# Kernel tuning notes

Hardware: AMD Instinct MI355X
Metric: run time of the kernel (lower is better)

The kernel has to match this reference:

```python
import jax, jax.numpy as jnp
from jax import lax
import numpy as np

INPUT_SIZE = 128
NUM_FRAMES = 4
NUM_OBJECTS = 32
DN = ('NCHW', 'OIHW', 'NCHW')


def _conv(x, w, b):
    y = lax.conv_general_dilated(x, w, window_strides=(1, 1), padding='SAME',
                                 dimension_numbers=DN)
    return y + b[None, :, None, None]


def setup_inputs() -> dict:
    key = jax.random.key(0)
    k = jax.random.split(key, 6)
    B = 32
    images = jax.random.uniform(k[0], (B, NUM_FRAMES, 3, INPUT_SIZE, INPUT_SIZE), jnp.float32) * 255.0
    rois = jax.random.randint(k[1], (B, INPUT_SIZE, INPUT_SIZE), 0, NUM_OBJECTS, jnp.int32)
    conv1_w = jax.random.normal(k[2], (64, 3 * NUM_FRAMES, 3, 3), jnp.float32) * 0.05
    conv1_b = jnp.zeros((64,), jnp.float32)
    conv2_w = jax.random.normal(k[3], (128, 64, 3, 3), jnp.float32) * 0.05
    conv2_b = jnp.zeros((128,), jnp.float32)
    return {'images': images, 'rois': rois, 'conv1_w': conv1_w, 'conv1_b': conv1_b,
            'conv2_w': conv2_w, 'conv2_b': conv2_b}


def reference(images, rois, conv1_w, conv1_b, conv2_w, conv2_b):
    B = images.shape[0]
    # backbone: conv -> relu -> maxpool2x2 -> conv -> relu
    x = images.reshape(B, 3 * NUM_FRAMES, INPUT_SIZE, INPUT_SIZE) / 255.0
    x = jax.nn.relu(_conv(x, conv1_w, conv1_b))
    x = lax.reduce_window(x, -jnp.inf, lax.max, (1, 1, 2, 2), (1, 1, 2, 2), 'VALID')
    x = jax.nn.relu(_conv(x, conv2_w, conv2_b))  # (B, 128, 64, 64)
    C = x.shape[1]
    # roi_pool: one-hot(rois) nearest-downsampled to 64x64, broadcast-multiply,
    # max over H,W == per-id segment max (x >= 0 post-relu; absent id -> 0)
    ids = rois[:, ::2, ::2].reshape(B, -1)
    feat = x.reshape(B, C, -1).transpose(0, 2, 1)  # (B, HW, C)

    def pool_one(f, i):  # f: (HW, C), i: (HW,)
        return jax.ops.segment_max(f, i, num_segments=NUM_OBJECTS)  # (O, C)

    pooled = jax.vmap(pool_one)(feat, ids)  # (B, O, C)
    return jnp.maximum(pooled, 0.0)
```

## Files before the change

kernel.cpp:

```cpp
#include <hip/hip_runtime.h>

#define IN 128
#define PD 64
#define C1 64
#define C2 128
#define ICC 12
#define NOBJ 32
#define PADW 66

typedef __attribute__((ext_vector_type(8))) short bf16x8;
typedef __attribute__((ext_vector_type(4))) float f32x4;

static __device__ __forceinline__ unsigned short f2bf(float f) {
  unsigned u = __float_as_uint(f);
  return (unsigned short)((u + 0x7FFFu + ((u >> 16) & 1u)) >> 16);
}

__global__ __launch_bounds__(256) void k0_pack_w1(
    const float* __restrict__ w1, unsigned short* __restrict__ wp)
{
  int i = blockIdx.x * 256 + threadIdx.x;
  if (i < 10 * C1 * 16) {
    int tap = i >> 10;
    int rem = i & 1023;
    int oc = rem >> 4, ch = rem & 15;
    float v = (tap < 9 && ch < ICC) ? w1[((size_t)oc * ICC + ch) * 9 + tap] : 0.f;
    wp[i] = f2bf(v);
  }
}

__global__ __launch_bounds__(512, 4) void k1_mfma(
    const float* __restrict__ img, const unsigned short* __restrict__ wp1,
    const float* __restrict__ b1, const float* __restrict__ w2,
    unsigned short* __restrict__ wq, unsigned short* __restrict__ xpad)
{
  const int t = threadIdx.x;

  if (blockIdx.y == 32) {
    for (int j = blockIdx.x * 512 + t; j < 9 * C2 * C1; j += 64 * 512) {
      const int tmp = j / 9, tap = j - tmp * 9;
      const int ic = tmp & 63, oc = tmp >> 6;
      const int k2 = ic >> 5, l16 = (ic >> 3) & 3, e = ic & 7;
      const int ocb = oc >> 4, l15 = oc & 15;
      wq[((tap * 2 + k2) * 8 + ocb) * 512 + l16 * 128 + l15 * 8 + e] = f2bf(w2[j]);
    }
    return;
  }

  const int l = t & 63, w = t >> 6;
  const int wm = w >> 1, wn = w & 1;
  const int bx = blockIdx.x & 7, by = blockIdx.x >> 3;
  const int b  = blockIdx.y;
  const int l15 = l & 15, l16 = l >> 4;

  __shared__ uint4 xs4[324 * 3];

  if (t < 324) {
    unsigned int* xu = reinterpret_cast<unsigned int*>(xs4);
    xu[t * 12 + 6] = 0;
    xu[t * 12 + 7] = 0;
  }

  const float* imgb = img + ((size_t)b * ICC << 14);
  float v0[4], v1[4];
  int   dpix[4], dcp[4];
#pragma unroll
  for (int it = 0; it < 4; ++it) {
    const int i = t + it * 512;
    const bool ok = i < 1944;
    const int cp  = ok ? (i / 324) : 0;
    const int pix = i - cp * 324;
    const int y = (pix * 57) >> 10;
    const int x = pix - y * 18;
    const int iy = by * 16 + y - 1, ix = bx * 16 + x - 1;
    dpix[it] = pix; dcp[it] = cp;
    v0[it] = 0.f; v1[it] = 0.f;
    if (ok && iy >= 0 && iy < IN && ix >= 0 && ix < IN) {
      const float* p0 = imgb + ((size_t)(2 * cp) << 14) + iy * IN + ix;
      v0[it] = p0[0];
      v1[it] = p0[16384];
    }
  }
#pragma unroll
  for (int it = 0; it < 4; ++it) {
    if (t + it * 512 < 1944) {
      unsigned short h0 = f2bf(v0[it] * (1.f / 255.f));
      unsigned short h1 = f2bf(v1[it] * (1.f / 255.f));
      reinterpret_cast<unsigned int*>(xs4)[dpix[it] * 12 + dcp[it]] =
          (unsigned int)h0 | ((unsigned int)h1 << 16);
    }
  }
  __syncthreads();

  f32x4 acc[4][2];
#pragma unroll
  for (int mf = 0; mf < 4; ++mf)
#pragma unroll
    for (int nf = 0; nf < 2; ++nf) acc[mf][nf] = (f32x4){0.f, 0.f, 0.f, 0.f};

  const char* xs_raw = reinterpret_cast<const char*>(xs4);
  const int ck = l16 & 1;
#pragma unroll
  for (int kp = 0; kp < 5; ++kp) {
    const int ta = 2 * kp, tb = 2 * kp + 1;
    const int tbA = (tb > 8) ? 8 : tb;
    const int dya = ta / 3, dxa = ta % 3;
    const int dyb = tbA / 3, dxb = tbA % 3;
    const int dy = (l16 < 2) ? dya : dyb;
    const int dx = (l16 < 2) ? dxa : dxb;
    const int tw = (l16 < 2) ? ta : tb;

    bf16x8 a[4], bw[2];
#pragma unroll
    for (int mf = 0; mf < 4; ++mf) {
      const int row = wm * 4 + mf;
      const int s = (row + dy) * 18 + (l15 + dx);
      a[mf] = *reinterpret_cast<const bf16x8*>(xs_raw + s * 48 + ck * 16);
    }
#pragma unroll
    for (int nf = 0; nf < 2; ++nf) {
      const int oc = wn * 32 + nf * 16 + l15;
      bw[nf] = *reinterpret_cast<const bf16x8*>(wp1 + ((tw * C1 + oc) * 16 + ck * 8));
    }
#pragma unroll
    for (int mf = 0; mf < 4; ++mf)
#pragma unroll
      for (int nf = 0; nf < 2; ++nf)
        acc[mf][nf] = __builtin_amdgcn_mfma_f32_16x16x32_bf16(
            a[mf], bw[nf], acc[mf][nf], 0, 0, 0);
  }

  float bias[2];
#pragma unroll
  for (int nf = 0; nf < 2; ++nf) bias[nf] = b1[wn * 32 + nf * 16 + l15];

#pragma unroll
  for (int q = 0; q < 2; ++q) {
    const int gy = by * 8 + wm * 2 + q;
    unsigned short* orow = xpad + (((size_t)b * PADW + (gy + 1)) * PADW + 1) * C1;
#pragma unroll
    for (int nf = 0; nf < 2; ++nf) {
      const int oc = wn * 32 + nf * 16 + l15;
      const f32x4 A0 = acc[2 * q][nf], A1 = acc[2 * q + 1][nf];
      const float p0 = fmaxf(fmaxf(A0[0], A0[1]), fmaxf(A1[0], A1[1]));
      const float p1 = fmaxf(fmaxf(A0[2], A0[3]), fmaxf(A1[2], A1[3]));
      const float v0s = fmaxf(p0 + bias[nf], 0.f);
      const float v1s = fmaxf(p1 + bias[nf], 0.f);
      const int gx0 = bx * 8 + l16 * 2;
      orow[(size_t)gx0 * C1 + oc]       = f2bf(v0s);
      orow[(size_t)(gx0 + 1) * C1 + oc] = f2bf(v1s);
    }
  }
}

__global__ __launch_bounds__(256) void k2_mfma(
    const unsigned short* __restrict__ xpad, const unsigned short* __restrict__ wq,
    const float* __restrict__ b2, const int* __restrict__ rois,
    float* __restrict__ part)
{
  const int t  = threadIdx.x;
  const int l  = t & 63, w = t >> 6;
  const int wm = w >> 1, wn = w & 1;
  const int bx = blockIdx.x & 3, by = blockIdx.x >> 2;
  const int b  = blockIdx.y;
  const int l15 = l & 15, l16 = l >> 4;

  __shared__ uint4 xs4[180 * 8];
  __shared__ int   smax[NOBJ * 132];
  __shared__ int   ids_s[128];

  const unsigned short* xb = xpad + (size_t)b * PADW * PADW * C1;
  uint4 sv[6];
#pragma unroll
  for (int it = 0; it < 6; ++it) {
    const int i = t + it * 256;
    const bool ok = i < 1440;
    const int r = i >> 3, ps = i & 7;
    const int y = (r * 57) >> 10;
    const int x = r - y * 18;
    const int cl = ps ^ (r & 7);
    const int gy = by * 8 + y, gx = bx * 16 + x;
    sv[it] = make_uint4(0, 0, 0, 0);
    if (ok && gy >= 1 && gy <= PD && gx >= 1 && gx <= PD)
      sv[it] = *(reinterpret_cast<const uint4*>(xb + ((size_t)gy * PADW + gx) * C1) + cl);
  }
#pragma unroll
  for (int it = 0; it < 6; ++it)
    if (t + it * 256 < 1440) xs4[t + it * 256] = sv[it];

  if (t < 128) {
    const int py = t >> 4, pxx = t & 15;
    ids_s[t] = rois[((size_t)b * IN + 2 * (by * 8 + py)) * IN + 2 * (bx * 16 + pxx)];
  }
  {
    uint4* sm4 = reinterpret_cast<uint4*>(smax);
    const uint4 z = make_uint4(0, 0, 0, 0);
#pragma unroll
    for (int i = 0; i < 5; ++i) {
      const int j = t + i * 256;
      if (j < 1056) sm4[j] = z;
    }
  }
  __syncthreads();

  f32x4 acc[4][4];
#pragma unroll
  for (int mf = 0; mf < 4; ++mf)
#pragma unroll
    for (int nf = 0; nf < 4; ++nf) acc[mf][nf] = (f32x4){0.f, 0.f, 0.f, 0.f};

  const char* xs_raw = reinterpret_cast<const char*>(xs4);

  bf16x8 aR[2][4], bR[2][4];
#pragma unroll
  for (int mf = 0; mf < 4; ++mf) {
    const int m_loc = wm * 64 + mf * 16 + l15;
    const int s = (m_loc >> 4) * 18 + (m_loc & 15);
    const int c = l16 ^ (s & 7);
    aR[0][mf] = *reinterpret_cast<const bf16x8*>(xs_raw + s * 128 + c * 16);
  }
#pragma unroll
  for (int nf = 0; nf < 4; ++nf)
    bR[0][nf] = *reinterpret_cast<const bf16x8*>(
        wq + ((size_t)(wn * 4 + nf)) * 512 + l * 8);

#pragma unroll
  for (int st = 0; st < 18; ++st) {
    const int cur = st & 1, nxt = cur ^ 1;
    if (st < 17) {
      const int s1 = st + 1;
      const int tap1 = s1 >> 1, k21 = s1 & 1;
      const int kr1 = tap1 / 3, kc1 = tap1 % 3;
#pragma unroll
      for (int nf = 0; nf < 4; ++nf)
        bR[nxt][nf] = *reinterpret_cast<const bf16x8*>(
            wq + ((size_t)((tap1 * 2 + k21) * 8 + wn * 4 + nf)) * 512 + l * 8);
#pragma unroll
      for (int mf = 0; mf < 4; ++mf) {
        const int m_loc = wm * 64 + mf * 16 + l15;
        const int s = ((m_loc >> 4) + kr1) * 18 + ((m_loc & 15) + kc1);
        const int c = (k21 * 4 + l16) ^ (s & 7);
        aR[nxt][mf] = *reinterpret_cast<const bf16x8*>(xs_raw + s * 128 + c * 16);
      }
    }
#pragma unroll
    for (int mf = 0; mf < 4; ++mf)
#pragma unroll
      for (int nf = 0; nf < 4; ++nf)
        acc[mf][nf] = __builtin_amdgcn_mfma_f32_16x16x32_bf16(
            aR[cur][mf], bR[cur][nf], acc[mf][nf], 0, 0, 0);
  }

  float bias[4];
#pragma unroll
  for (int nf = 0; nf < 4; ++nf) bias[nf] = b2[wn * 64 + nf * 16 + l15];

#pragma unroll
  for (int mf = 0; mf < 4; ++mf) {
#pragma unroll
    for (int reg = 0; reg < 4; ++reg) {
      const int m_loc = wm * 64 + mf * 16 + l16 * 4 + reg;
      const int id = ids_s[m_loc];
#pragma unroll
      for (int nf = 0; nf < 4; ++nf) {
        const int oc = wn * 64 + nf * 16 + l15;
        const float val = fmaxf(acc[mf][nf][reg] + bias[nf], 0.f);
        atomicMax(&smax[id * 132 + oc], __float_as_int(val));
      }
    }
  }
  __syncthreads();

  uint4* pb4 = reinterpret_cast<uint4*>(part + ((size_t)b * 32 + blockIdx.x) * (NOBJ * C2));
  const uint4* sm4 = reinterpret_cast<const uint4*>(smax);
#pragma unroll
  for (int i = 0; i < 4; ++i) {
    const int j = t + i * 256;
    const int row = j >> 5, c4 = j & 31;
    pb4[j] = sm4[row * 33 + c4];
  }
}

__global__ __launch_bounds__(256) void k3_reduce(
    const float* __restrict__ part, float* __restrict__ out)
{
  const int idx = blockIdx.x * 256 + threadIdx.x;
  const int b = idx >> 12, slot = idx & 4095;
  const float* p = part + (size_t)b * 32 * 4096 + slot;
  float m = 0.f;
#pragma unroll
  for (int tl = 0; tl < 32; ++tl) m = fmaxf(m, p[tl * 4096]);
  out[idx] = m;
}

extern "C" void kernel_launch(void* const* d_in, const int* in_sizes, int n_in,
                              void* d_out, int out_size, void* d_ws, size_t ws_size,
                              hipStream_t stream)
{
  (void)in_sizes; (void)n_in; (void)ws_size; (void)out_size;
  const float* images = (const float*)d_in[0];
  const int*   rois   = (const int*)d_in[1];
  const float* w1     = (const float*)d_in[2];
  const float* b1     = (const float*)d_in[3];
  const float* w2     = (const float*)d_in[4];
  const float* b2     = (const float*)d_in[5];

  const size_t xpad_bytes = (size_t)32 * PADW * PADW * C1 * 2;
  const size_t wq_bytes   = (size_t)9 * C2 * C1 * 2;
  const size_t wp1_bytes  = (size_t)10 * C1 * 16 * 2;

  unsigned short* xpad = (unsigned short*)d_ws;
  unsigned short* wq   = (unsigned short*)((char*)d_ws + xpad_bytes);
  unsigned short* wp1  = (unsigned short*)((char*)d_ws + xpad_bytes + wq_bytes);
  float* part = (float*)((char*)d_ws + xpad_bytes + wq_bytes + wp1_bytes);

  hipLaunchKernelGGL(k0_pack_w1, dim3(40), dim3(256), 0, stream, w1, wp1);

  hipLaunchKernelGGL(k1_mfma, dim3(64, 33), dim3(512), 0, stream,
                     images, wp1, b1, w2, wq, xpad);

  hipLaunchKernelGGL(k2_mfma, dim3(32, 32), dim3(256), 0, stream,
                     xpad, wq, b2, rois, part);

  hipLaunchKernelGGL(k3_reduce, dim3(512), dim3(256), 0, stream,
                     part, (float*)d_out);
}
```

Before: 56.51 us.

## Switch both conv MFMA kernels from 16x16x32 to 32x32x16 bf16 tiles

Both convolution kernels now use the 32x32x16 bf16 MFMA instruction instead of 16x16x32, and the packed weight layouts for conv1 and conv2 are reorganised to match the new operand fragments. Conv1 now does one tap per K-step, dropping the old paired-tap trick and its padding tap. Conv2 runs 36 smaller K-steps with fewer fragments per wave. The intent is fewer LDS operand loads and MFMA issues per output tile, at the cost of redoing the accumulator-to-pixel mapping used by the pooling and atomic-max epilogues.

```diff
diff --git a/kernel.cpp b/kernel.cpp
--- a/kernel.cpp
+++ b/kernel.cpp
@@ -9,7 +9,7 @@
 #define PADW 66
 
 typedef __attribute__((ext_vector_type(8))) short bf16x8;
-typedef __attribute__((ext_vector_type(4))) float f32x4;
+typedef __attribute__((ext_vector_type(16))) float f32x16;
 
 static __device__ __forceinline__ unsigned short f2bf(float f) {
   unsigned u = __float_as_uint(f);
@@ -19,13 +19,13 @@
 __global__ __launch_bounds__(256) void k0_pack_w1(
     const float* __restrict__ w1, unsigned short* __restrict__ wp)
 {
-  int i = blockIdx.x * 256 + threadIdx.x;
-  if (i < 10 * C1 * 16) {
-    int tap = i >> 10;
-    int rem = i & 1023;
-    int oc = rem >> 4, ch = rem & 15;
-    float v = (tap < 9 && ch < ICC) ? w1[((size_t)oc * ICC + ch) * 9 + tap] : 0.f;
-    wp[i] = f2bf(v);
+  int j = blockIdx.x * 256 + threadIdx.x;
+  if (j < 9 * 2 * 64 * 8) {
+    const int e = j & 7, lane = (j >> 3) & 63, ocb = (j >> 9) & 1, tap = j >> 10;
+    const int oc = ocb * 32 + (lane & 31);
+    const int ch = (lane >> 5) * 8 + e;
+    float v = (ch < ICC) ? w1[((size_t)oc * ICC + ch) * 9 + tap] : 0.f;
+    wp[j] = f2bf(v);
   }
 }
 
@@ -40,9 +40,11 @@
     for (int j = blockIdx.x * 512 + t; j < 9 * C2 * C1; j += 64 * 512) {
       const int tmp = j / 9, tap = j - tmp * 9;
       const int ic = tmp & 63, oc = tmp >> 6;
-      const int k2 = ic >> 5, l16 = (ic >> 3) & 3, e = ic & 7;
-      const int ocb = oc >> 4, l15 = oc & 15;
-      wq[((tap * 2 + k2) * 8 + ocb) * 512 + l16 * 128 + l15 * 8 + e] = f2bf(w2[j]);
+      const int s  = tap * 4 + (ic >> 4);
+      const int kk = ic & 15;
+      const int lane = ((kk >> 3) << 5) | (oc & 31);
+      const int ocb  = oc >> 5;
+      wq[((s * 4 + ocb) << 9) + lane * 8 + (kk & 7)] = f2bf(w2[j]);
     }
     return;
   }
@@ -51,7 +53,7 @@
   const int wm = w >> 1, wn = w & 1;
   const int bx = blockIdx.x & 7, by = blockIdx.x >> 3;
   const int b  = blockIdx.y;
-  const int l15 = l & 15, l16 = l >> 4;
+  const int l31 = l & 31, h = l >> 5;
 
   __shared__ uint4 xs4[324 * 3];
 
@@ -92,63 +94,42 @@
   }
   __syncthreads();
 
-  f32x4 acc[4][2];
-#pragma unroll
-  for (int mf = 0; mf < 4; ++mf)
-#pragma unroll
-    for (int nf = 0; nf < 2; ++nf) acc[mf][nf] = (f32x4){0.f, 0.f, 0.f, 0.f};
+  f32x16 acc[2];
+#pragma unroll
+  for (int mf = 0; mf < 2; ++mf)
+#pragma unroll
+    for (int e = 0; e < 16; ++e) acc[mf][e] = 0.f;
 
   const char* xs_raw = reinterpret_cast<const char*>(xs4);
-  const int ck = l16 & 1;
-#pragma unroll
-  for (int kp = 0; kp < 5; ++kp) {
-    const int ta = 2 * kp, tb = 2 * kp + 1;
-    const int tbA = (tb > 8) ? 8 : tb;
-    const int dya = ta / 3, dxa = ta % 3;
-    const int dyb = tbA / 3, dxb = tbA % 3;
-    const int dy = (l16 < 2) ? dya : dyb;
-    const int dx = (l16 < 2) ? dxa : dxb;
-    const int tw = (l16 < 2) ? ta : tb;
-
-    bf16x8 a[4], bw[2];
-#pragma unroll
-    for (int mf = 0; mf < 4; ++mf) {
-      const int row = wm * 4 + mf;
-      const int s = (row + dy) * 18 + (l15 + dx);
-      a[mf] = *reinterpret_cast<const bf16x8*>(xs_raw + s * 48 + ck * 16);
-    }
-#pragma unroll
-    for (int nf = 0; nf < 2; ++nf) {
-      const int oc = wn * 32 + nf * 16 + l15;
-      bw[nf] = *reinterpret_cast<const bf16x8*>(wp1 + ((tw * C1 + oc) * 16 + ck * 8));
-    }
-#pragma unroll
-    for (int mf = 0; mf < 4; ++mf)
-#pragma unroll
-      for (int nf = 0; nf < 2; ++nf)
-        acc[mf][nf] = __builtin_amdgcn_mfma_f32_16x16x32_bf16(
-            a[mf], bw[nf], acc[mf][nf], 0, 0, 0);
-  }
-
-  float bias[2];
-#pragma unroll
-  for (int nf = 0; nf < 2; ++nf) bias[nf] = b1[wn * 32 + nf * 16 + l15];
-
-#pragma unroll
-  for (int q = 0; q < 2; ++q) {
-    const int gy = by * 8 + wm * 2 + q;
+#pragma unroll
+  for (int tap = 0; tap < 9; ++tap) {
+    const int dy = tap / 3, dx = tap % 3;
+    bf16x8 bw = *reinterpret_cast<const bf16x8*>(wp1 + (((tap * 2 + wn) << 9) + l * 8));
+    bf16x8 a[2];
+#pragma unroll
+    for (int mf = 0; mf < 2; ++mf) {
+      const int m  = wm * 64 + mf * 32 + l31;
+      const int s  = ((m >> 4) + dy) * 18 + ((m & 15) + dx);
+      a[mf] = *reinterpret_cast<const bf16x8*>(xs_raw + s * 48 + h * 16);
+    }
+#pragma unroll
+    for (int mf = 0; mf < 2; ++mf)
+      acc[mf] = __builtin_amdgcn_mfma_f32_32x32x16_bf16(a[mf], bw, acc[mf], 0, 0, 0);
+  }
+
+  const int oc = wn * 32 + l31;
+  const float bias0 = b1[oc];
+#pragma unroll
+  for (int mf = 0; mf < 2; ++mf) {
+    const int gy = by * 8 + wm * 2 + mf;
     unsigned short* orow = xpad + (((size_t)b * PADW + (gy + 1)) * PADW + 1) * C1;
 #pragma unroll
-    for (int nf = 0; nf < 2; ++nf) {
-      const int oc = wn * 32 + nf * 16 + l15;
-      const f32x4 A0 = acc[2 * q][nf], A1 = acc[2 * q + 1][nf];
-      const float p0 = fmaxf(fmaxf(A0[0], A0[1]), fmaxf(A1[0], A1[1]));
-      const float p1 = fmaxf(fmaxf(A0[2], A0[3]), fmaxf(A1[2], A1[3]));
-      const float v0s = fmaxf(p0 + bias[nf], 0.f);
-      const float v1s = fmaxf(p1 + bias[nf], 0.f);
-      const int gx0 = bx * 8 + l16 * 2;
-      orow[(size_t)gx0 * C1 + oc]       = f2bf(v0s);
-      orow[(size_t)(gx0 + 1) * C1 + oc] = f2bf(v1s);
+    for (int j = 0; j < 4; ++j) {
+      const float p = fmaxf(fmaxf(acc[mf][2 * j], acc[mf][2 * j + 1]),
+                            fmaxf(acc[mf][2 * j + 8], acc[mf][2 * j + 9]));
+      const float v = fmaxf(p + bias0, 0.f);
+      const int gx = bx * 8 + ((j & 1) | ((j >> 1) << 2)) + 2 * h;
+      orow[(size_t)gx * C1 + oc] = f2bf(v);
     }
   }
 }
@@ -163,7 +144,7 @@
   const int wm = w >> 1, wn = w & 1;
   const int bx = blockIdx.x & 3, by = blockIdx.x >> 2;
   const int b  = blockIdx.y;
-  const int l15 = l & 15, l16 = l >> 4;
+  const int l31 = l & 31, h = l >> 5;
 
   __shared__ uint4 xs4[180 * 8];
   __shared__ int   smax[NOBJ * 132];
@@ -203,67 +184,70 @@
   }
   __syncthreads();
 
-  f32x4 acc[4][4];
-#pragma unroll
-  for (int mf = 0; mf < 4; ++mf)
-#pragma unroll
-    for (int nf = 0; nf < 4; ++nf) acc[mf][nf] = (f32x4){0.f, 0.f, 0.f, 0.f};
+  f32x16 acc[2][2];
+#pragma unroll
+  for (int mf = 0; mf < 2; ++mf)
+#pragma unroll
+    for (int nf = 0; nf < 2; ++nf)
+#pragma unroll
+      for (int e = 0; e < 16; ++e) acc[mf][nf][e] = 0.f;
 
   const char* xs_raw = reinterpret_cast<const char*>(xs4);
 
-  bf16x8 aR[2][4], bR[2][4];
-#pragma unroll
-  for (int mf = 0; mf < 4; ++mf) {
-    const int m_loc = wm * 64 + mf * 16 + l15;
-    const int s = (m_loc >> 4) * 18 + (m_loc & 15);
-    const int c = l16 ^ (s & 7);
-    aR[0][mf] = *reinterpret_cast<const bf16x8*>(xs_raw + s * 128 + c * 16);
-  }
-#pragma unroll
-  for (int nf = 0; nf < 4; ++nf)
+  bf16x8 aR[2][2], bR[2][2];
+#pragma unroll
+  for (int mf = 0; mf < 2; ++mf) {
+    const int m = wm * 64 + mf * 32 + l31;
+    const int sp = (m >> 4) * 18 + (m & 15);
+    const int c = h ^ (sp & 7);
+    aR[0][mf] = *reinterpret_cast<const bf16x8*>(xs_raw + sp * 128 + c * 16);
+  }
+#pragma unroll
+  for (int nf = 0; nf < 2; ++nf)
     bR[0][nf] = *reinterpret_cast<const bf16x8*>(
-        wq + ((size_t)(wn * 4 + nf)) * 512 + l * 8);
-
-#pragma unroll
-  for (int st = 0; st < 18; ++st) {
+        wq + (((size_t)(wn * 2 + nf)) << 9) + l * 8);
+
+#pragma unroll
+  for (int st = 0; st < 36; ++st) {
     const int cur = st & 1, nxt = cur ^ 1;
-    if (st < 17) {
+    if (st < 35) {
       const int s1 = st + 1;
-      const int tap1 = s1 >> 1, k21 = s1 & 1;
+      const int tap1 = s1 >> 2, q1 = s1 & 3;
       const int kr1 = tap1 / 3, kc1 = tap1 % 3;
 #pragma unroll
-      for (int nf = 0; nf < 4; ++nf)
+      for (int nf = 0; nf < 2; ++nf)
         bR[nxt][nf] = *reinterpret_cast<const bf16x8*>(
-            wq + ((size_t)((tap1 * 2 + k21) * 8 + wn * 4 + nf)) * 512 + l * 8);
-#pragma unroll
-      for (int mf = 0; mf < 4; ++mf) {
-        const int m_loc = wm * 64 + mf * 16 + l15;
-        const int s = ((m_loc >> 4) + kr1) * 18 + ((m_loc & 15) + kc1);
-        const int c = (k21 * 4 + l16) ^ (s & 7);
-        aR[nxt][mf] = *reinterpret_cast<const bf16x8*>(xs_raw + s * 128 + c * 16);
+            wq + (((size_t)(s1 * 4 + wn * 2 + nf)) << 9) + l * 8);
+#pragma unroll
+      for (int mf = 0; mf < 2; ++mf) {
+        const int m = wm * 64 + mf * 32 + l31;
+        const int sp = ((m >> 4) + kr1) * 18 + ((m & 15) + kc1);
+        const int c = (q1 * 2 + h) ^ (sp & 7);
+        aR[nxt][mf] = *reinterpret_cast<const bf16x8*>(xs_raw + sp * 128 + c * 16);
       }
     }
 #pragma unroll
-    for (int mf = 0; mf < 4; ++mf)
-#pragma unroll
-      for (int nf = 0; nf < 4; ++nf)
-        acc[mf][nf] = __builtin_amdgcn_mfma_f32_16x16x32_bf16(
+    for (int mf = 0; mf < 2; ++mf)
+#pragma unroll
+      for (int nf = 0; nf < 2; ++nf)
+        acc[mf][nf] = __builtin_amdgcn_mfma_f32_32x32x16_bf16(
             aR[cur][mf], bR[cur][nf], acc[mf][nf], 0, 0, 0);
   }
 
-  float bias[4];
-#pragma unroll
-  for (int nf = 0; nf < 4; ++nf) bias[nf] = b2[wn * 64 + nf * 16 + l15];
-
-#pragma unroll
-  for (int mf = 0; mf < 4; ++mf) {
-#pragma unroll
-    for (int reg = 0; reg < 4; ++reg) {
-      const int m_loc = wm * 64 + mf * 16 + l16 * 4 + reg;
-      const int id = ids_s[m_loc];
-#pragma unroll
-      for (int nf = 0; nf < 4; ++nf) {
-        const int oc = wn * 64 + nf * 16 + l15;
+  float bias[2];
+#pragma unroll
+  for (int nf = 0; nf < 2; ++nf) bias[nf] = b2[wn * 64 + nf * 32 + l31];
+
+#pragma unroll
+  for (int mf = 0; mf < 2; ++mf) {
+#pragma unroll
+    for (int reg = 0; reg < 16; ++reg) {
+      const int row = (reg & 3) + 8 * (reg >> 2) + 4 * h;
+      const int pix = wm * 64 + mf * 32 + row;
+      const int id = ids_s[pix];
+#pragma unroll
+      for (int nf = 0; nf < 2; ++nf) {
+        const int oc = wn * 64 + nf * 32 + l31;
         const float val = fmaxf(acc[mf][nf][reg] + bias[nf], 0.f);
         atomicMax(&smax[id * 132 + oc], __float_as_int(val));
       }
@@ -306,15 +290,15 @@
   const float* b2     = (const float*)d_in[5];
 
   const size_t xpad_bytes = (size_t)32 * PADW * PADW * C1 * 2;
-  const size_t wq_bytes   = (size_t)9 * C2 * C1 * 2;
-  const size_t wp1_bytes  = (size_t)10 * C1 * 16 * 2;
+  const size_t wq_bytes   = (size_t)36 * 4 * 512 * 2;
+  const size_t wp1_bytes  = (size_t)9 * 2 * 512 * 2;
 
   unsigned short* xpad = (unsigned short*)d_ws;
   unsigned short* wq   = (unsigned short*)((char*)d_ws + xpad_bytes);
   unsigned short* wp1  = (unsigned short*)((char*)d_ws + xpad_bytes + wq_bytes);
   float* part = (float*)((char*)d_ws + xpad_bytes + wq_bytes + wp1_bytes);
 
-  hipLaunchKernelGGL(k0_pack_w1, dim3(40), dim3(256), 0, stream, w1, wp1);
+  hipLaunchKernelGGL(k0_pack_w1, dim3(36), dim3(256), 0, stream, w1, wp1);
 
   hipLaunchKernelGGL(k1_mfma, dim3(64, 33), dim3(512), 0, stream,
                      images, wp1, b1, w2, wq, xpad);
```

Result: slower. 61.07 us (+8.1%).

## Process two horizontal tiles per conv1 block with prefetched image loads

Applied to the files above, without the earlier changes.

Each conv1 block now handles two adjacent 16x16 tiles instead of one, so the grid is halved. The global image loads for the second tile are issued before the first tile's MFMA and epilogue, hiding load latency behind compute. The trade-offs are fewer blocks in flight, extra register pressure from holding the prefetched values, and one more barrier per block. The weight-repack stride is adjusted to match the smaller grid.

```diff
diff --git a/kernel.cpp b/kernel.cpp
--- a/kernel.cpp
+++ b/kernel.cpp
@@ -37,7 +37,7 @@
   const int t = threadIdx.x;
 
   if (blockIdx.y == 32) {
-    for (int j = blockIdx.x * 512 + t; j < 9 * C2 * C1; j += 64 * 512) {
+    for (int j = blockIdx.x * 512 + t; j < 9 * C2 * C1; j += 32 * 512) {
       const int tmp = j / 9, tap = j - tmp * 9;
       const int ic = tmp & 63, oc = tmp >> 6;
       const int k2 = ic >> 5, l16 = (ic >> 3) & 3, e = ic & 7;
@@ -49,8 +49,9 @@
 
   const int l = t & 63, w = t >> 6;
   const int wm = w >> 1, wn = w & 1;
-  const int bx = blockIdx.x & 7, by = blockIdx.x >> 3;
-  const int b  = blockIdx.y;
+  const int bxp = (blockIdx.x & 3) << 1;
+  const int by  = blockIdx.x >> 2;
+  const int b   = blockIdx.y;
   const int l15 = l & 15, l16 = l >> 4;
 
   __shared__ uint4 xs4[324 * 3];
@@ -62,95 +63,123 @@
   }
 
   const float* imgb = img + ((size_t)b * ICC << 14);
-  float v0[4], v1[4];
-  int   dpix[4], dcp[4];
-#pragma unroll
-  for (int it = 0; it < 4; ++it) {
-    const int i = t + it * 512;
-    const bool ok = i < 1944;
-    const int cp  = ok ? (i / 324) : 0;
-    const int pix = i - cp * 324;
-    const int y = (pix * 57) >> 10;
-    const int x = pix - y * 18;
-    const int iy = by * 16 + y - 1, ix = bx * 16 + x - 1;
-    dpix[it] = pix; dcp[it] = cp;
-    v0[it] = 0.f; v1[it] = 0.f;
-    if (ok && iy >= 0 && iy < IN && ix >= 0 && ix < IN) {
-      const float* p0 = imgb + ((size_t)(2 * cp) << 14) + iy * IN + ix;
-      v0[it] = p0[0];
-      v1[it] = p0[16384];
-    }
-  }
-#pragma unroll
-  for (int it = 0; it < 4; ++it) {
-    if (t + it * 512 < 1944) {
-      unsigned short h0 = f2bf(v0[it] * (1.f / 255.f));
-      unsigned short h1 = f2bf(v1[it] * (1.f / 255.f));
-      reinterpret_cast<unsigned int*>(xs4)[dpix[it] * 12 + dcp[it]] =
-          (unsigned int)h0 | ((unsigned int)h1 << 16);
-    }
-  }
-  __syncthreads();
-
-  f32x4 acc[4][2];
-#pragma unroll
-  for (int mf = 0; mf < 4; ++mf)
-#pragma unroll
-    for (int nf = 0; nf < 2; ++nf) acc[mf][nf] = (f32x4){0.f, 0.f, 0.f, 0.f};
+
+  auto stage_load = [&](int bx, float (&v0)[4], float (&v1)[4]) {
+#pragma unroll
+    for (int it = 0; it < 4; ++it) {
+      const int i = t + it * 512;
+      const bool ok = i < 1944;
+      const int cp  = ok ? (i / 324) : 0;
+      const int pix = i - cp * 324;
+      const int y = (pix * 57) >> 10;
+      const int x = pix - y * 18;
+      const int iy = by * 16 + y - 1, ix = bx * 16 + x - 1;
+      v0[it] = 0.f; v1[it] = 0.f;
+      if (ok && iy >= 0 && iy < IN && ix >= 0 && ix < IN) {
+        const float* p0 = imgb + ((size_t)(2 * cp) << 14) + iy * IN + ix;
+        v0[it] = p0[0];
+        v1[it] = p0[16384];
+      }
+    }
+  };
+  auto stage_write = [&](const float (&v0)[4], const float (&v1)[4]) {
+#pragma unroll
+    for (int it = 0; it < 4; ++it) {
+      const int i = t + it * 512;
+      if (i < 1944) {
+        const int cp  = i / 324;
+        const int pix = i - cp * 324;
+        unsigned short h0 = f2bf(v0[it] * (1.f / 255.f));
+        unsigned short h1 = f2bf(v1[it] * (1.f / 255.f));
+        reinterpret_cast<unsigned int*>(xs4)[pix * 12 + cp] =
+            (unsigned int)h0 | ((unsigned int)h1 << 16);
+      }
+    }
+  };
 
   const char* xs_raw = reinterpret_cast<const char*>(xs4);
   const int ck = l16 & 1;
-#pragma unroll
-  for (int kp = 0; kp < 5; ++kp) {
-    const int ta = 2 * kp, tb = 2 * kp + 1;
-    const int tbA = (tb > 8) ? 8 : tb;
-    const int dya = ta / 3, dxa = ta % 3;
-    const int dyb = tbA / 3, dxb = tbA % 3;
-    const int dy = (l16 < 2) ? dya : dyb;
-    const int dx = (l16 < 2) ? dxa : dxb;
-    const int tw = (l16 < 2) ? ta : tb;
-
-    bf16x8 a[4], bw[2];
-#pragma unroll
-    for (int mf = 0; mf < 4; ++mf) {
-      const int row = wm * 4 + mf;
-      const int s = (row + dy) * 18 + (l15 + dx);
-      a[mf] = *reinterpret_cast<const bf16x8*>(xs_raw + s * 48 + ck * 16);
-    }
-#pragma unroll
-    for (int nf = 0; nf < 2; ++nf) {
-      const int oc = wn * 32 + nf * 16 + l15;
-      bw[nf] = *reinterpret_cast<const bf16x8*>(wp1 + ((tw * C1 + oc) * 16 + ck * 8));
-    }
-#pragma unroll
-    for (int mf = 0; mf < 4; ++mf)
-#pragma unroll
-      for (int nf = 0; nf < 2; ++nf)
-        acc[mf][nf] = __builtin_amdgcn_mfma_f32_16x16x32_bf16(
-            a[mf], bw[nf], acc[mf][nf], 0, 0, 0);
-  }
+
+  auto do_mfma = [&](f32x4 (&acc)[4][2]) {
+#pragma unroll
+    for (int kp = 0; kp < 5; ++kp) {
+      const int ta = 2 * kp, tb = 2 * kp + 1;
+      const int tbA = (tb > 8) ? 8 : tb;
+      const int dya = ta / 3, dxa = ta % 3;
+      const int dyb = tbA / 3, dxb = tbA % 3;
+      const int dy = (l16 < 2) ? dya : dyb;
+      const int dx = (l16 < 2) ? dxa : dxb;
+      const int tw = (l16 < 2) ? ta : tb;
+
+      bf16x8 a[4], bw[2];
+#pragma unroll
+      for (int mf = 0; mf < 4; ++mf) {
+        const int row = wm * 4 + mf;
+        const int s = (row + dy) * 18 + (l15 + dx);
+        a[mf] = *reinterpret_cast<const bf16x8*>(xs_raw + s * 48 + ck * 16);
+      }
+#pragma unroll
+      for (int nf = 0; nf < 2; ++nf) {
+        const int oc = wn * 32 + nf * 16 + l15;
+        bw[nf] = *reinterpret_cast<const bf16x8*>(wp1 + ((tw * C1 + oc) * 16 + ck * 8));
+      }
+#pragma unroll
+      for (int mf = 0; mf < 4; ++mf)
+#pragma unroll
+        for (int nf = 0; nf < 2; ++nf)
+          acc[mf][nf] = __builtin_amdgcn_mfma_f32_16x16x32_bf16(
+              a[mf], bw[nf], acc[mf][nf], 0, 0, 0);
+    }
+  };
 
   float bias[2];
 #pragma unroll
   for (int nf = 0; nf < 2; ++nf) bias[nf] = b1[wn * 32 + nf * 16 + l15];
 
-#pragma unroll
-  for (int q = 0; q < 2; ++q) {
-    const int gy = by * 8 + wm * 2 + q;
-    unsigned short* orow = xpad + (((size_t)b * PADW + (gy + 1)) * PADW + 1) * C1;
-#pragma unroll
-    for (int nf = 0; nf < 2; ++nf) {
-      const int oc = wn * 32 + nf * 16 + l15;
-      const f32x4 A0 = acc[2 * q][nf], A1 = acc[2 * q + 1][nf];
-      const float p0 = fmaxf(fmaxf(A0[0], A0[1]), fmaxf(A1[0], A1[1]));
-      const float p1 = fmaxf(fmaxf(A0[2], A0[3]), fmaxf(A1[2], A1[3]));
-      const float v0s = fmaxf(p0 + bias[nf], 0.f);
-      const float v1s = fmaxf(p1 + bias[nf], 0.f);
-      const int gx0 = bx * 8 + l16 * 2;
-      orow[(size_t)gx0 * C1 + oc]       = f2bf(v0s);
-      orow[(size_t)(gx0 + 1) * C1 + oc] = f2bf(v1s);
-    }
-  }
+  auto epilogue = [&](int bx, f32x4 (&acc)[4][2]) {
+#pragma unroll
+    for (int q = 0; q < 2; ++q) {
+      const int gy = by * 8 + wm * 2 + q;
+      unsigned short* orow = xpad + (((size_t)b * PADW + (gy + 1)) * PADW + 1) * C1;
+#pragma unroll
+      for (int nf = 0; nf < 2; ++nf) {
+        const int oc = wn * 32 + nf * 16 + l15;
+        const f32x4 A0 = acc[2 * q][nf], A1 = acc[2 * q + 1][nf];
+        const float p0 = fmaxf(fmaxf(A0[0], A0[1]), fmaxf(A1[0], A1[1]));
+        const float p1 = fmaxf(fmaxf(A0[2], A0[3]), fmaxf(A1[2], A1[3]));
+        const float v0s = fmaxf(p0 + bias[nf], 0.f);
+        const float v1s = fmaxf(p1 + bias[nf], 0.f);
+        const int gx0 = bx * 8 + l16 * 2;
+        orow[(size_t)gx0 * C1 + oc]       = f2bf(v0s);
+        orow[(size_t)(gx0 + 1) * C1 + oc] = f2bf(v1s);
+      }
+    }
+  };
+
+  float v0[4], v1[4];
+  f32x4 acc[4][2];
+
+  stage_load(bxp, v0, v1);
+  stage_write(v0, v1);
+  __syncthreads();
+
+  stage_load(bxp + 1, v0, v1);
+#pragma unroll
+  for (int mf = 0; mf < 4; ++mf)
+#pragma unroll
+    for (int nf = 0; nf < 2; ++nf) acc[mf][nf] = (f32x4){0.f, 0.f, 0.f, 0.f};
+  do_mfma(acc);
+  epilogue(bxp, acc);
+  __syncthreads();
+
+  stage_write(v0, v1);
+  __syncthreads();
+#pragma unroll
+  for (int mf = 0; mf < 4; ++mf)
+#pragma unroll
+    for (int nf = 0; nf < 2; ++nf) acc[mf][nf] = (f32x4){0.f, 0.f, 0.f, 0.f};
+  do_mfma(acc);
+  epilogue(bxp + 1, acc);
 }
 
 __global__ __launch_bounds__(256) void k2_mfma(
@@ -316,7 +345,7 @@
 
   hipLaunchKernelGGL(k0_pack_w1, dim3(40), dim3(256), 0, stream, w1, wp1);
 
-  hipLaunchKernelGGL(k1_mfma, dim3(64, 33), dim3(512), 0, stream,
+  hipLaunchKernelGGL(k1_mfma, dim3(32, 33), dim3(512), 0, stream,
                      images, wp1, b1, w2, wq, xpad);
 
   hipLaunchKernelGGL(k2_mfma, dim3(32, 32), dim3(256), 0, stream,
```

Result: slower. 57.83 us (+2.3%).

## Double conv2 spatial tile per block to 16x16 and halve partial reductions

Applied to the files above, without the earlier changes.

The conv2 MFMA kernel now computes a 16x16 output pixel tile per block instead of 8x16. Each wave handles 8 M-fragments, which doubles reuse of every weight fragment and shrinks the halo overhead relative to the tile. The grid and the partial-max buffer shrink by half, so the final reduction reads half as much data. In exchange, the register double-buffering prefetch of A and B fragments is removed, accumulator register pressure doubles, LDS use grows to about 58KB per block, and fewer blocks are launched, which may lower occupancy and latency hiding.

```diff
diff --git a/kernel.cpp b/kernel.cpp
--- a/kernel.cpp
+++ b/kernel.cpp
@@ -165,32 +165,29 @@
   const int b  = blockIdx.y;
   const int l15 = l & 15, l16 = l >> 4;
 
-  __shared__ uint4 xs4[180 * 8];
+  __shared__ uint4 xs4[324 * 8];
   __shared__ int   smax[NOBJ * 132];
-  __shared__ int   ids_s[128];
+  __shared__ int   ids_s[256];
 
   const unsigned short* xb = xpad + (size_t)b * PADW * PADW * C1;
-  uint4 sv[6];
-#pragma unroll
-  for (int it = 0; it < 6; ++it) {
+#pragma unroll
+  for (int it = 0; it < 11; ++it) {
     const int i = t + it * 256;
-    const bool ok = i < 1440;
-    const int r = i >> 3, ps = i & 7;
-    const int y = (r * 57) >> 10;
-    const int x = r - y * 18;
-    const int cl = ps ^ (r & 7);
-    const int gy = by * 8 + y, gx = bx * 16 + x;
-    sv[it] = make_uint4(0, 0, 0, 0);
-    if (ok && gy >= 1 && gy <= PD && gx >= 1 && gx <= PD)
-      sv[it] = *(reinterpret_cast<const uint4*>(xb + ((size_t)gy * PADW + gx) * C1) + cl);
-  }
-#pragma unroll
-  for (int it = 0; it < 6; ++it)
-    if (t + it * 256 < 1440) xs4[t + it * 256] = sv[it];
-
-  if (t < 128) {
+    if (i < 2592) {
+      const int r = i >> 3, ps = i & 7;
+      const int y = (r * 57) >> 10;
+      const int x = r - y * 18;
+      const int cl = ps ^ (r & 7);
+      const int gy = by * 16 + y, gx = bx * 16 + x;
+      uint4 v = make_uint4(0, 0, 0, 0);
+      if (gy >= 1 && gy <= PD && gx >= 1 && gx <= PD)
+        v = *(reinterpret_cast<const uint4*>(xb + ((size_t)gy * PADW + gx) * C1) + cl);
+      xs4[i] = v;
+    }
+  }
+  {
     const int py = t >> 4, pxx = t & 15;
-    ids_s[t] = rois[((size_t)b * IN + 2 * (by * 8 + py)) * IN + 2 * (bx * 16 + pxx)];
+    ids_s[t] = rois[((size_t)b * IN + 2 * (by * 16 + py)) * IN + 2 * (bx * 16 + pxx)];
   }
   {
     uint4* sm4 = reinterpret_cast<uint4*>(smax);
@@ -203,52 +200,36 @@
   }
   __syncthreads();
 
-  f32x4 acc[4][4];
-#pragma unroll
-  for (int mf = 0; mf < 4; ++mf)
+  f32x4 acc[8][4];
+#pragma unroll
+  for (int mf = 0; mf < 8; ++mf)
 #pragma unroll
     for (int nf = 0; nf < 4; ++nf) acc[mf][nf] = (f32x4){0.f, 0.f, 0.f, 0.f};
 
   const char* xs_raw = reinterpret_cast<const char*>(xs4);
 
-  bf16x8 aR[2][4], bR[2][4];
-#pragma unroll
-  for (int mf = 0; mf < 4; ++mf) {
-    const int m_loc = wm * 64 + mf * 16 + l15;
-    const int s = (m_loc >> 4) * 18 + (m_loc & 15);
-    const int c = l16 ^ (s & 7);
-    aR[0][mf] = *reinterpret_cast<const bf16x8*>(xs_raw + s * 128 + c * 16);
-  }
-#pragma unroll
-  for (int nf = 0; nf < 4; ++nf)
-    bR[0][nf] = *reinterpret_cast<const bf16x8*>(
-        wq + ((size_t)(wn * 4 + nf)) * 512 + l * 8);
-
 #pragma unroll
   for (int st = 0; st < 18; ++st) {
-    const int cur = st & 1, nxt = cur ^ 1;
-    if (st < 17) {
-      const int s1 = st + 1;
-      const int tap1 = s1 >> 1, k21 = s1 & 1;
-      const int kr1 = tap1 / 3, kc1 = tap1 % 3;
-#pragma unroll
-      for (int nf = 0; nf < 4; ++nf)
-        bR[nxt][nf] = *reinterpret_cast<const bf16x8*>(
-            wq + ((size_t)((tap1 * 2 + k21) * 8 + wn * 4 + nf)) * 512 + l * 8);
-#pragma unroll
-      for (int mf = 0; mf < 4; ++mf) {
-        const int m_loc = wm * 64 + mf * 16 + l15;
-        const int s = ((m_loc >> 4) + kr1) * 18 + ((m_loc & 15) + kc1);
-        const int c = (k21 * 4 + l16) ^ (s & 7);
-        aR[nxt][mf] = *reinterpret_cast<const bf16x8*>(xs_raw + s * 128 + c * 16);
-      }
-    }
-#pragma unroll
-    for (int mf = 0; mf < 4; ++mf)
+    const int tap = st >> 1, k21 = st & 1;
+    const int kr = tap / 3, kc = tap % 3;
+    bf16x8 a[8], bw[4];
+#pragma unroll
+    for (int mf = 0; mf < 8; ++mf) {
+      const int m_loc = wm * 128 + mf * 16 + l15;
+      const int s = ((m_loc >> 4) + kr) * 18 + ((m_loc & 15) + kc);
+      const int c = (k21 * 4 + l16) ^ (s & 7);
+      a[mf] = *reinterpret_cast<const bf16x8*>(xs_raw + s * 128 + c * 16);
+    }
+#pragma unroll
+    for (int nf = 0; nf < 4; ++nf)
+      bw[nf] = *reinterpret_cast<const bf16x8*>(
+          wq + ((size_t)((tap * 2 + k21) * 8 + wn * 4 + nf)) * 512 + l * 8);
+#pragma unroll
+    for (int mf = 0; mf < 8; ++mf)
 #pragma unroll
       for (int nf = 0; nf < 4; ++nf)
         acc[mf][nf] = __builtin_amdgcn_mfma_f32_16x16x32_bf16(
-            aR[cur][mf], bR[cur][nf], acc[mf][nf], 0, 0, 0);
+            a[mf], bw[nf], acc[mf][nf], 0, 0, 0);
   }
 
   float bias[4];
@@ -256,10 +237,10 @@
   for (int nf = 0; nf < 4; ++nf) bias[nf] = b2[wn * 64 + nf * 16 + l15];
 
 #pragma unroll
-  for (int mf = 0; mf < 4; ++mf) {
+  for (int mf = 0; mf < 8; ++mf) {
 #pragma unroll
     for (int reg = 0; reg < 4; ++reg) {
-      const int m_loc = wm * 64 + mf * 16 + l16 * 4 + reg;
+      const int m_loc = wm * 128 + mf * 16 + l16 * 4 + reg;
       const int id = ids_s[m_loc];
 #pragma unroll
       for (int nf = 0; nf < 4; ++nf) {
@@ -271,7 +252,7 @@
   }
   __syncthreads();
 
-  uint4* pb4 = reinterpret_cast<uint4*>(part + ((size_t)b * 32 + blockIdx.x) * (NOBJ * C2));
+  uint4* pb4 = reinterpret_cast<uint4*>(part + ((size_t)b * 16 + blockIdx.x) * (NOBJ * C2));
   const uint4* sm4 = reinterpret_cast<const uint4*>(smax);
 #pragma unroll
   for (int i = 0; i < 4; ++i) {
@@ -286,10 +267,10 @@
 {
   const int idx = blockIdx.x * 256 + threadIdx.x;
   const int b = idx >> 12, slot = idx & 4095;
-  const float* p = part + (size_t)b * 32 * 4096 + slot;
+  const float* p = part + (size_t)b * 16 * 4096 + slot;
   float m = 0.f;
 #pragma unroll
-  for (int tl = 0; tl < 32; ++tl) m = fmaxf(m, p[tl * 4096]);
+  for (int tl = 0; tl < 16; ++tl) m = fmaxf(m, p[tl * 4096]);
   out[idx] = m;
 }
 
@@ -319,7 +300,7 @@
   hipLaunchKernelGGL(k1_mfma, dim3(64, 33), dim3(512), 0, stream,
                      images, wp1, b1, w2, wq, xpad);
 
-  hipLaunchKernelGGL(k2_mfma, dim3(32, 32), dim3(256), 0, stream,
+  hipLaunchKernelGGL(k2_mfma, dim3(16, 32), dim3(256), 0, stream,
                      xpad, wq, b2, rois, part);
 
   hipLaunchKernelGGL(k3_reduce, dim3(512), dim3(256), 0, stream,
```

Result: slower. 63.37 us (+12.1%).
